# Optimization experiments

Hardware: AMD Instinct MI355X
Metric: run time of the kernel (lower is better)

Reference implementation:

```python
import jax, jax.numpy as jnp
import numpy as np

N = 5000
NFEAT = 512
NHID = 64
NHEADS = 8
NCLASS = 40
ALPHA = 0.2  # leaky relu slope
NEG_INF = -9e15


def setup_inputs() -> dict:
    key = jax.random.key(0)
    ks = jax.random.split(key, 12)
    x = jax.random.normal(ks[0], (N, NFEAT), dtype=jnp.float32)
    # binary adjacency, ~32 avg degree, with self loops
    adj = (jax.random.uniform(ks[1], (N, N)) < (32.0 / N)).astype(jnp.float32)
    adj = jnp.maximum(adj, jnp.eye(N, dtype=jnp.float32))
    s = 1.0 / np.sqrt(NFEAT)
    W_h = jax.random.uniform(ks[2], (NHEADS, NFEAT, NHID), minval=-s, maxval=s, dtype=jnp.float32)
    a_h = jax.random.uniform(ks[3], (NHEADS, 2 * NHID), minval=-s, maxval=s, dtype=jnp.float32)
    s2 = 1.0 / np.sqrt(NHID * NHEADS)
    W_o = jax.random.uniform(ks[4], (NHID * NHEADS, NHID), minval=-s2, maxval=s2, dtype=jnp.float32)
    a_o = jax.random.uniform(ks[5], (2 * NHID,), minval=-s2, maxval=s2, dtype=jnp.float32)
    s3 = 1.0 / np.sqrt(NHID)
    fc1_w = jax.random.uniform(ks[6], (NHID, 200), minval=-s3, maxval=s3, dtype=jnp.float32)
    fc1_b = jax.random.uniform(ks[7], (200,), minval=-s3, maxval=s3, dtype=jnp.float32)
    s4 = 1.0 / np.sqrt(200)
    fc2_w = jax.random.uniform(ks[8], (200, NCLASS), minval=-s4, maxval=s4, dtype=jnp.float32)
    fc2_b = jax.random.uniform(ks[9], (NCLASS,), minval=-s4, maxval=s4, dtype=jnp.float32)
    return {"x": x, "adj": adj, "W_h": W_h, "a_h": a_h, "W_o": W_o, "a_o": a_o,
            "fc1_w": fc1_w, "fc1_b": fc1_b, "fc2_w": fc2_w, "fc2_b": fc2_b}


def _masked_attention(e, adj):
    # e: [..., N, N]; mask where adj == 0, then row softmax
    e = jnp.where(adj > 0, e, NEG_INF)
    return jax.nn.softmax(e, axis=-1)


def reference(x, adj, W_h, a_h, W_o, a_o, fc1_w, fc1_b, fc2_w, fc2_b):
    # ---- multi-head GAT layer (concat=True), eval mode (dropout off) ----
    Wh = jnp.einsum('nf,hfo->hno', x, W_h)                 # [H, N, nhid]
    f1 = jnp.einsum('hno,ho->hn', Wh, a_h[:, :NHID])       # [H, N]
    f2 = jnp.einsum('hno,ho->hn', Wh, a_h[:, NHID:])       # [H, N]
    e = jax.nn.leaky_relu(f1[:, :, None] + f2[:, None, :], ALPHA)  # [H, N, N]
    att = _masked_attention(e, adj[None, :, :])
    h = jnp.einsum('hnm,hmo->hno', att, Wh)                # [H, N, nhid]
    h1 = jax.nn.elu(h).transpose(1, 0, 2).reshape(N, NHEADS * NHID)  # concat heads

    # ---- output GAT layer (concat=False) ----
    Wh2 = h1 @ W_o                                         # [N, nhid]
    g1 = Wh2 @ a_o[:NHID]                                  # [N]
    g2 = Wh2 @ a_o[NHID:]                                  # [N]
    e2 = jax.nn.leaky_relu(g1[:, None] + g2[None, :], ALPHA)
    att2 = _masked_attention(e2, adj)
    h2 = att2 @ Wh2                                        # [N, nhid]

    # ---- MLP head ----
    h3 = jax.nn.elu(h2 @ fc1_w + fc1_b)
    return h3 @ fc2_w + fc2_b                              # [N, nclass]
```

## Files before the change

kernel.cpp:

```cpp
#include <hip/hip_runtime.h>

typedef unsigned short u16;
typedef unsigned int u32;
typedef unsigned long long u64;
typedef __bf16 bf16_t;
typedef __bf16 bf16x8 __attribute__((ext_vector_type(8)));
typedef float f32x4 __attribute__((ext_vector_type(4)));

#define NN 5000
#define NF 512
#define NH 64
#define HEADS 8
#define NCLS 40
#define CAP 128
#define LRELU 0.2f

#define SCAN_BLKS 1250
#define CVT_AB_BLKS 344
#define PREP2_GRID (SCAN_BLKS + CVT_AB_BLKS + 8)

__device__ __forceinline__ bool adj_is_bf16(const void* adj) {
    return ((*(const u32*)adj) & 0xFFFFu) != 0u;
}
__device__ __forceinline__ u16 rne_bf16(float f) {
    u32 u = __float_as_uint(f);
    u += 0x7FFFu + ((u >> 16) & 1u);
    return (u16)(u >> 16);
}
__device__ __forceinline__ float up_bf16(u16 h) {
    return __uint_as_float((u32)h << 16);
}

__global__ __launch_bounds__(256) void prep2(const void* __restrict__ adj,
                                             const void* __restrict__ x, const void* __restrict__ W_h,
                                             const void* a_h, const void* W_o, const void* a_o,
                                             const void* f1w, const void* f1b,
                                             const void* f2w, const void* f2b,
                                             int* __restrict__ nbr, int* __restrict__ deg,
                                             u16* __restrict__ xc, u16* __restrict__ whc,
                                             float* a_hc, float* W_oc, float* a_oc,
                                             float* f1wc, float* f1bc, float* f2wc, float* f2bc) {
    const bool isb = adj_is_bf16(adj);
    const int b = blockIdx.x;
    if (b < SCAN_BLKS) {
        const int lane = threadIdx.x & 63;
        const int wid  = threadIdx.x >> 6;
        const int n = b * 4 + wid;
        int* nrow = nbr + (size_t)n * CAP;
        const u64 lt = (1ull << lane) - 1;
        int total = 0;
        if (!isb) {
            const uint4* row4 = (const uint4*)((const float*)adj + (size_t)n * NN);
            #pragma unroll
            for (int pass = 0; pass < 2; ++pass) {
                uint4 v[10];
                #pragma unroll
                for (int k = 0; k < 10; ++k) {
                    int c = (pass * 10 + k) * 64 + lane;
                    v[k] = (c < 1250) ? row4[c] : make_uint4(0u, 0u, 0u, 0u);
                }
                #pragma unroll
                for (int k = 0; k < 10; ++k) {
                    int c = (pass * 10 + k) * 64 + lane;
                    u32 w[4] = {v[k].x, v[k].y, v[k].z, v[k].w};
                    #pragma unroll
                    for (int j = 0; j < 4; ++j) {
                        bool nz = w[j] != 0u;
                        u64 m = __ballot(nz);
                        if (nz) {
                            int pos = total + __popcll(m & lt);
                            if (pos < CAP) nrow[pos] = c * 4 + j;
                        }
                        total += __popcll(m);
                    }
                }
            }
        } else {
            const uint4* row4 = (const uint4*)((const u16*)adj + (size_t)n * NN);
            #pragma unroll
            for (int pass = 0; pass < 2; ++pass) {
                uint4 v[5];
                #pragma unroll
                for (int k = 0; k < 5; ++k) {
                    int c = (pass * 5 + k) * 64 + lane;
                    v[k] = (c < 625) ? row4[c] : make_uint4(0u, 0u, 0u, 0u);
                }
                #pragma unroll
                for (int k = 0; k < 5; ++k) {
                    int c = (pass * 5 + k) * 64 + lane;
                    u32 w[4] = {v[k].x, v[k].y, v[k].z, v[k].w};
                    #pragma unroll
                    for (int j = 0; j < 4; ++j) {
                        bool nz = (w[j] & 0xFFFFu) != 0u;
                        u64 m = __ballot(nz);
                        if (nz) {
                            int pos = total + __popcll(m & lt);
                            if (pos < CAP) nrow[pos] = c * 8 + 2 * j;
                        }
                        total += __popcll(m);
                        bool nz2 = (w[j] >> 16) != 0u;
                        u64 m2 = __ballot(nz2);
                        if (nz2) {
                            int pos = total + __popcll(m2 & lt);
                            if (pos < CAP) nrow[pos] = c * 8 + 2 * j + 1;
                        }
                        total += __popcll(m2);
                    }
                }
            }
        }
        if (lane == 0) deg[n] = total < CAP ? total : CAP;
    } else if (b < SCAN_BLKS + CVT_AB_BLKS) {
        const int total = NN * NF + HEADS * NF * NH;
        for (int i = (b - SCAN_BLKS) * 256 + threadIdx.x; i < total; i += CVT_AB_BLKS * 256) {
            const void* src; u16* dst; int off;
            if (i < NN * NF) { src = x; dst = xc; off = i; }
            else             { src = W_h; dst = whc; off = i - NN * NF; }
            dst[off] = isb ? ((const u16*)src)[off] : rne_bf16(((const float*)src)[off]);
        }
    } else {
        const int s0 = HEADS * 2 * NH, s1 = HEADS * NH * NH, s2 = 2 * NH,
                  s3 = NH * 200, s4 = 200, s5 = 200 * NCLS, s6 = NCLS;
        const int total = s0 + s1 + s2 + s3 + s4 + s5 + s6;
        for (int i = (b - SCAN_BLKS - CVT_AB_BLKS) * 256 + threadIdx.x; i < total; i += 8 * 256) {
            const void* src; float* dst; int off = i;
            if (off < s0) { src = a_h; dst = a_hc; }
            else if ((off -= s0) < s1) { src = W_o;  dst = W_oc; }
            else if ((off -= s1) < s2) { src = a_o;  dst = a_oc; }
            else if ((off -= s2) < s3) { src = f1w;  dst = f1wc; }
            else if ((off -= s3) < s4) { src = f1b;  dst = f1bc; }
            else if ((off -= s4) < s5) { src = f2w;  dst = f2wc; }
            else { off -= s5;           src = f2b;  dst = f2bc; }
            dst[off] = isb ? up_bf16(((const u16*)src)[off]) : ((const float*)src)[off];
        }
    }
}

__global__ __launch_bounds__(256) void gemm1_f(const bf16_t* __restrict__ x,
                                               const bf16_t* __restrict__ W_h,
                                               const float* __restrict__ a_h,
                                               float* __restrict__ Wh,
                                               float* __restrict__ f1,
                                               float* __restrict__ f2) {
    const int lane = threadIdx.x & 63;
    const int wid  = threadIdx.x >> 6;
    const int rg = blockIdx.x;
    const int h  = blockIdx.y;
    const int quad = lane >> 4;
    const int lr   = lane & 15;
    const int kq   = quad * 8;
    const int nCol = wid * 16 + lr;
    const bf16_t* Bh = W_h + (size_t)h * NF * NH;
    __shared__ float f1s[4][64], f2s[4][64];

    bf16x8 bfrag[16];
    #pragma unroll
    for (int s = 0; s < 16; ++s) {
        bf16x8 bb;
        #pragma unroll
        for (int j = 0; j < 8; ++j) bb[j] = Bh[(s * 32 + kq + j) * NH + nCol];
        bfrag[s] = bb;
    }
    const float a1c = a_h[h * 128 + nCol];
    const float a2c = a_h[h * 128 + NH + nCol];

    for (int t = 0; t < 4; ++t) {
        const int rb = rg * 64 + t * 16;
        int row  = rb + lr;
        int rowc = row < NN ? row : NN - 1;
        const bf16_t* xp = x + (size_t)rowc * NF + kq;
        f32x4 acc = {0.f, 0.f, 0.f, 0.f};
        #pragma unroll
        for (int s = 0; s < 16; ++s) {
            bf16x8 a = *(const bf16x8*)(xp + s * 32);
            acc = __builtin_amdgcn_mfma_f32_16x16x32_bf16(a, bfrag[s], acc, 0, 0, 0);
        }
        #pragma unroll
        for (int r = 0; r < 4; ++r) {
            int gr = rb + quad * 4 + r;
            if (gr < NN) Wh[((size_t)(h * NN + gr)) * NH + nCol] = acc[r];
            float p1 = acc[r] * a1c, p2 = acc[r] * a2c;
            #pragma unroll
            for (int o = 8; o; o >>= 1) { p1 += __shfl_xor(p1, o); p2 += __shfl_xor(p2, o); }
            if (lr == 0) { f1s[wid][t * 16 + quad * 4 + r] = p1; f2s[wid][t * 16 + quad * 4 + r] = p2; }
        }
    }
    __syncthreads();
    if (wid == 0) {
        int gr = rg * 64 + lane;
        if (gr < NN) {
            f1[h * NN + gr] = f1s[0][lane] + f1s[1][lane] + f1s[2][lane] + f1s[3][lane];
            f2[h * NN + gr] = f2s[0][lane] + f2s[1][lane] + f2s[2][lane] + f2s[3][lane];
        }
    }
}

__global__ __launch_bounds__(256) void agg1(const float* __restrict__ Wh,
                                            const float* __restrict__ f1,
                                            const float* __restrict__ f2,
                                            const int* __restrict__ nbr,
                                            const int* __restrict__ deg,
                                            float* __restrict__ h1) {
    const int lane = threadIdx.x & 63;
    const int wid  = threadIdx.x >> 6;
    const int gw = blockIdx.x * 4 + wid;
    const int h = gw / NN;
    const int n = gw - h * NN;
    __shared__ float s_alpha[4][CAP];
    __shared__ int   s_nbr[4][CAP];
    const int d = deg[n];
    const int* nb = nbr + (size_t)n * CAP;
    const float f1n = f1[gw];
    const float* f2h = f2 + (size_t)h * NN;

    float mx = -INFINITY;
    for (int j = lane; j < d; j += 64) {
        int m = nb[j];
        s_nbr[wid][j] = m;
        float e = f1n + f2h[m];
        e = e > 0.f ? e : LRELU * e;
        s_alpha[wid][j] = e;
        mx = fmaxf(mx, e);
    }
    #pragma unroll
    for (int o = 32; o; o >>= 1) mx = fmaxf(mx, __shfl_xor(mx, o));
    float sm = 0.f;
    for (int j = lane; j < d; j += 64) {
        float p = expf(s_alpha[wid][j] - mx);
        s_alpha[wid][j] = p;
        sm += p;
    }
    #pragma unroll
    for (int o = 32; o; o >>= 1) sm += __shfl_xor(sm, o);

    float acc0 = 0.f, acc1 = 0.f, acc2 = 0.f, acc3 = 0.f;
    const float* WhL = Wh + (size_t)h * NN * NH + lane;
    int j = 0;
    for (; j + 4 <= d; j += 4) {
        acc0 += s_alpha[wid][j]     * WhL[(size_t)s_nbr[wid][j]     * NH];
        acc1 += s_alpha[wid][j + 1] * WhL[(size_t)s_nbr[wid][j + 1] * NH];
        acc2 += s_alpha[wid][j + 2] * WhL[(size_t)s_nbr[wid][j + 2] * NH];
        acc3 += s_alpha[wid][j + 3] * WhL[(size_t)s_nbr[wid][j + 3] * NH];
    }
    for (; j < d; ++j) acc0 += s_alpha[wid][j] * WhL[(size_t)s_nbr[wid][j] * NH];
    float hv = (acc0 + acc1 + acc2 + acc3) / sm;
    hv = hv > 0.f ? hv : expf(hv) - 1.f;
    h1[(size_t)n * (HEADS * NH) + h * NH + lane] = hv;
}

__global__ __launch_bounds__(256) void gemm2_4(const float* __restrict__ h1,
                                               const float* __restrict__ W_o,
                                               const float* __restrict__ a_o,
                                               float* __restrict__ Wh2,
                                               float* __restrict__ g1,
                                               float* __restrict__ g2) {
    const int t = threadIdx.x;
    const int n0 = blockIdx.x * 4;
    __shared__ float sh[4 * 512];
    __shared__ float ps[4][4][64];
    const float4* src = (const float4*)(h1 + (size_t)n0 * 512);
    ((float4*)sh)[t]       = src[t];
    ((float4*)sh)[t + 256] = src[t + 256];
    __syncthreads();
    const int o = t & 63, part = t >> 6;
    float a0 = 0.f, a1 = 0.f, a2 = 0.f, a3 = 0.f;
    const float* wo = W_o + part * 128 * 64 + o;
    const float* s0 = sh + part * 128;
    #pragma unroll 4
    for (int f = 0; f < 128; ++f) {
        float w = wo[f * 64];
        a0 += s0[f] * w; a1 += s0[512 + f] * w; a2 += s0[1024 + f] * w; a3 += s0[1536 + f] * w;
    }
    ps[part][0][o] = a0; ps[part][1][o] = a1; ps[part][2][o] = a2; ps[part][3][o] = a3;
    __syncthreads();
    const int nd = t >> 6;
    float w2 = ps[0][nd][o] + ps[1][nd][o] + ps[2][nd][o] + ps[3][nd][o];
    Wh2[(size_t)(n0 + nd) * 64 + o] = w2;
    float p1 = w2 * a_o[o], p2 = w2 * a_o[64 + o];
    #pragma unroll
    for (int s = 32; s; s >>= 1) { p1 += __shfl_xor(p1, s); p2 += __shfl_xor(p2, s); }
    if (o == 0) { g1[n0 + nd] = p1; g2[n0 + nd] = p2; }
}

__global__ __launch_bounds__(256) void agg2_mlp(const float* __restrict__ Wh2,
                                                const float* __restrict__ g1,
                                                const float* __restrict__ g2,
                                                const int* __restrict__ nbr,
                                                const int* __restrict__ deg,
                                                const float* __restrict__ fc1_w,
                                                const float* __restrict__ fc1_b,
                                                const float* __restrict__ fc2_w,
                                                const float* __restrict__ fc2_b,
                                                float* __restrict__ out) {
    const int lane = threadIdx.x & 63;
    const int wid  = threadIdx.x >> 6;
    const int t = threadIdx.x;
    const int n0 = blockIdx.x * 4;
    const int n = n0 + wid;
    __shared__ float s_alpha[4][CAP];
    __shared__ int   s_nbr[4][CAP];
    __shared__ float s_h2[4][NH];
    __shared__ float s_h3[4][200];
    __shared__ float ps2[2][4][NCLS];
    const int d = deg[n];
    const int* nb = nbr + (size_t)n * CAP;
    const float gn = g1[n];

    float mx = -INFINITY;
    for (int j = lane; j < d; j += 64) {
        int m = nb[j];
        s_nbr[wid][j] = m;
        float e = gn + g2[m];
        e = e > 0.f ? e : LRELU * e;
        s_alpha[wid][j] = e;
        mx = fmaxf(mx, e);
    }
    #pragma unroll
    for (int o = 32; o; o >>= 1) mx = fmaxf(mx, __shfl_xor(mx, o));
    float sm = 0.f;
    for (int j = lane; j < d; j += 64) {
        float p = expf(s_alpha[wid][j] - mx);
        s_alpha[wid][j] = p;
        sm += p;
    }
    #pragma unroll
    for (int o = 32; o; o >>= 1) sm += __shfl_xor(sm, o);

    float acc0 = 0.f, acc1 = 0.f, acc2 = 0.f, acc3 = 0.f;
    int j = 0;
    for (; j + 4 <= d; j += 4) {
        acc0 += s_alpha[wid][j]     * Wh2[(size_t)s_nbr[wid][j]     * NH + lane];
        acc1 += s_alpha[wid][j + 1] * Wh2[(size_t)s_nbr[wid][j + 1] * NH + lane];
        acc2 += s_alpha[wid][j + 2] * Wh2[(size_t)s_nbr[wid][j + 2] * NH + lane];
        acc3 += s_alpha[wid][j + 3] * Wh2[(size_t)s_nbr[wid][j + 3] * NH + lane];
    }
    for (; j < d; ++j) acc0 += s_alpha[wid][j] * Wh2[(size_t)s_nbr[wid][j] * NH + lane];
    s_h2[wid][lane] = (acc0 + acc1 + acc2 + acc3) / sm;
    __syncthreads();

    if (t < 200) {
        float b0 = 0.f, b1 = 0.f, b2 = 0.f, b3 = 0.f;
        #pragma unroll 4
        for (int f = 0; f < NH; ++f) {
            float w = fc1_w[f * 200 + t];
            b0 += s_h2[0][f] * w; b1 += s_h2[1][f] * w; b2 += s_h2[2][f] * w; b3 += s_h2[3][f] * w;
        }
        float bb = fc1_b[t];
        b0 += bb; b1 += bb; b2 += bb; b3 += bb;
        s_h3[0][t] = b0 > 0.f ? b0 : expf(b0) - 1.f;
        s_h3[1][t] = b1 > 0.f ? b1 : expf(b1) - 1.f;
        s_h3[2][t] = b2 > 0.f ? b2 : expf(b2) - 1.f;
        s_h3[3][t] = b3 > 0.f ? b3 : expf(b3) - 1.f;
    }
    __syncthreads();

    if (t < 80) {
        const int o = t % 40, fh = t / 40;
        float c0 = 0.f, c1 = 0.f, c2 = 0.f, c3 = 0.f;
        #pragma unroll 4
        for (int f = fh * 100; f < fh * 100 + 100; ++f) {
            float w = fc2_w[f * NCLS + o];
            c0 += s_h3[0][f] * w; c1 += s_h3[1][f] * w; c2 += s_h3[2][f] * w; c3 += s_h3[3][f] * w;
        }
        ps2[fh][0][o] = c0; ps2[fh][1][o] = c1; ps2[fh][2][o] = c2; ps2[fh][3][o] = c3;
    }
    __syncthreads();
    if (t < 160) {
        const int nd = t / 40, o = t % 40;
        out[(size_t)(n0 + nd) * NCLS + o] = ps2[0][nd][o] + ps2[1][nd][o] + fc2_b[o];
    }
}

extern "C" void kernel_launch(void* const* d_in, const int* in_sizes, int n_in,
                              void* d_out, int out_size, void* d_ws, size_t ws_size,
                              hipStream_t stream) {
    const void* x     = d_in[0];
    const void* adj   = d_in[1];
    const void* W_h   = d_in[2];
    const void* a_h   = d_in[3];
    const void* W_o   = d_in[4];
    const void* a_o   = d_in[5];
    const void* fc1_w = d_in[6];
    const void* fc1_b = d_in[7];
    const void* fc2_w = d_in[8];
    const void* fc2_b = d_in[9];
    float* out = (float*)d_out;

    char* ws = (char*)d_ws;
    int*   nbr   = (int*)(ws + 0);
    int*   deg   = (int*)(ws + 2560000);
    float* Wh    = (float*)(ws + 2580000);
    float* f1    = (float*)(ws + 12820000);
    float* f2    = (float*)(ws + 12980000);
    float* h1    = (float*)(ws + 13140000);
    float* Wh2   = (float*)(ws + 23380000);
    float* g1    = (float*)(ws + 24660000);
    float* g2    = (float*)(ws + 24680000);
    u16*   xc    = (u16*)(ws + 24700000);
    u16*   whc   = (u16*)(ws + 29820000);
    float* a_hc  = (float*)(ws + 30344288);
    float* W_oc  = (float*)(ws + 30348384);
    float* a_oc  = (float*)(ws + 30479456);
    float* f1wc  = (float*)(ws + 30479968);
    float* f1bc  = (float*)(ws + 30531168);
    float* f2wc  = (float*)(ws + 30531968);
    float* f2bc  = (float*)(ws + 30563968);

    prep2<<<PREP2_GRID, 256, 0, stream>>>(adj, x, W_h, a_h, W_o, a_o,
                                          fc1_w, fc1_b, fc2_w, fc2_b,
                                          nbr, deg, xc, whc, a_hc, W_oc, a_oc,
                                          f1wc, f1bc, f2wc, f2bc);
    gemm1_f<<<dim3(79, HEADS), 256, 0, stream>>>((const bf16_t*)xc, (const bf16_t*)whc,
                                                 a_hc, Wh, f1, f2);
    agg1<<<HEADS * NN / 4, 256, 0, stream>>>(Wh, f1, f2, nbr, deg, h1);
    gemm2_4<<<NN / 4, 256, 0, stream>>>(h1, W_oc, a_oc, Wh2, g1, g2);
    agg2_mlp<<<NN / 4, 256, 0, stream>>>(Wh2, g1, g2, nbr, deg,
                                         f1wc, f1bc, f2wc, f2bc, out);
}
```

Baseline: 283.2 us.

## Fuse adjacency scan into first-layer aggregation and vectorize input conversion

Moves the dense adjacency row scan out of the prep kernel and into the first-layer aggregation kernel. Each block now handles one node, with its four waves scanning quarters of the row and merging the neighbor lists in shared memory. Those lists are shared across all eight heads and still written to global memory for the second layer. The bf16 conversion of x and W_h now processes four elements per thread with nontemporal loads. The 100MB adjacency read now happens in a kernel that runs after the GEMM, which lengthens that kernel's critical path, and the node-per-block split leaves only two heads per wave.

Result: no change. 282.7 us (-0.2%).

```diff
diff --git a/kernel.cpp b/kernel.cpp
--- a/kernel.cpp
+++ b/kernel.cpp
@@ -6,6 +6,7 @@
 typedef __bf16 bf16_t;
 typedef __bf16 bf16x8 __attribute__((ext_vector_type(8)));
 typedef float f32x4 __attribute__((ext_vector_type(4)));
+typedef u32 u32x4 __attribute__((ext_vector_type(4)));
 
 #define NN 5000
 #define NF 512
@@ -15,9 +16,8 @@
 #define CAP 128
 #define LRELU 0.2f
 
-#define SCAN_BLKS 1250
-#define CVT_AB_BLKS 344
-#define PREP2_GRID (SCAN_BLKS + CVT_AB_BLKS + 8)
+#define CVT_BIG 320
+#define CVT_GRID (CVT_BIG + 8)
 
 __device__ __forceinline__ bool adj_is_bf16(const void* adj) {
     return ((*(const u32*)adj) & 0xFFFFu) != 0u;
@@ -30,99 +30,42 @@
 __device__ __forceinline__ float up_bf16(u16 h) {
     return __uint_as_float((u32)h << 16);
 }
-
-__global__ __launch_bounds__(256) void prep2(const void* __restrict__ adj,
-                                             const void* __restrict__ x, const void* __restrict__ W_h,
-                                             const void* a_h, const void* W_o, const void* a_o,
-                                             const void* f1w, const void* f1b,
-                                             const void* f2w, const void* f2b,
-                                             int* __restrict__ nbr, int* __restrict__ deg,
-                                             u16* __restrict__ xc, u16* __restrict__ whc,
-                                             float* a_hc, float* W_oc, float* a_oc,
-                                             float* f1wc, float* f1bc, float* f2wc, float* f2bc) {
+__device__ __forceinline__ u32x4 ntload4(const void* p, int idx) {
+    return __builtin_nontemporal_load(((const u32x4*)p) + idx);
+}
+
+__global__ __launch_bounds__(256) void cvt(const void* __restrict__ x, const void* __restrict__ W_h,
+                                           const void* __restrict__ adj,
+                                           const void* a_h, const void* W_o, const void* a_o,
+                                           const void* f1w, const void* f1b,
+                                           const void* f2w, const void* f2b,
+                                           u16* __restrict__ xc, u16* __restrict__ whc,
+                                           float* a_hc, float* W_oc, float* a_oc,
+                                           float* f1wc, float* f1bc, float* f2wc, float* f2bc) {
     const bool isb = adj_is_bf16(adj);
     const int b = blockIdx.x;
-    if (b < SCAN_BLKS) {
-        const int lane = threadIdx.x & 63;
-        const int wid  = threadIdx.x >> 6;
-        const int n = b * 4 + wid;
-        int* nrow = nbr + (size_t)n * CAP;
-        const u64 lt = (1ull << lane) - 1;
-        int total = 0;
-        if (!isb) {
-            const uint4* row4 = (const uint4*)((const float*)adj + (size_t)n * NN);
-            #pragma unroll
-            for (int pass = 0; pass < 2; ++pass) {
-                uint4 v[10];
-                #pragma unroll
-                for (int k = 0; k < 10; ++k) {
-                    int c = (pass * 10 + k) * 64 + lane;
-                    v[k] = (c < 1250) ? row4[c] : make_uint4(0u, 0u, 0u, 0u);
-                }
-                #pragma unroll
-                for (int k = 0; k < 10; ++k) {
-                    int c = (pass * 10 + k) * 64 + lane;
-                    u32 w[4] = {v[k].x, v[k].y, v[k].z, v[k].w};
-                    #pragma unroll
-                    for (int j = 0; j < 4; ++j) {
-                        bool nz = w[j] != 0u;
-                        u64 m = __ballot(nz);
-                        if (nz) {
-                            int pos = total + __popcll(m & lt);
-                            if (pos < CAP) nrow[pos] = c * 4 + j;
-                        }
-                        total += __popcll(m);
-                    }
-                }
+    if (b < CVT_BIG) {
+        const int X4 = NN * NF / 4;
+        const int T4 = X4 + HEADS * NF * NH / 4;
+        for (int i = b * 256 + threadIdx.x; i < T4; i += CVT_BIG * 256) {
+            const void* src; u16* dst; int off;
+            if (i < X4) { src = x; dst = xc; off = i; }
+            else        { src = W_h; dst = whc; off = i - X4; }
+            ushort4 o;
+            if (isb) {
+                o = ((const ushort4*)src)[off];
+            } else {
+                u32x4 vv = ntload4(src, off);
+                o.x = rne_bf16(__uint_as_float(vv[0])); o.y = rne_bf16(__uint_as_float(vv[1]));
+                o.z = rne_bf16(__uint_as_float(vv[2])); o.w = rne_bf16(__uint_as_float(vv[3]));
             }
-        } else {
-            const uint4* row4 = (const uint4*)((const u16*)adj + (size_t)n * NN);
-            #pragma unroll
-            for (int pass = 0; pass < 2; ++pass) {
-                uint4 v[5];
-                #pragma unroll
-                for (int k = 0; k < 5; ++k) {
-                    int c = (pass * 5 + k) * 64 + lane;
-                    v[k] = (c < 625) ? row4[c] : make_uint4(0u, 0u, 0u, 0u);
-                }
-                #pragma unroll
-                for (int k = 0; k < 5; ++k) {
-                    int c = (pass * 5 + k) * 64 + lane;
-                    u32 w[4] = {v[k].x, v[k].y, v[k].z, v[k].w};
-                    #pragma unroll
-                    for (int j = 0; j < 4; ++j) {
-                        bool nz = (w[j] & 0xFFFFu) != 0u;
-                        u64 m = __ballot(nz);
-                        if (nz) {
-                            int pos = total + __popcll(m & lt);
-                            if (pos < CAP) nrow[pos] = c * 8 + 2 * j;
-                        }
-                        total += __popcll(m);
-                        bool nz2 = (w[j] >> 16) != 0u;
-                        u64 m2 = __ballot(nz2);
-                        if (nz2) {
-                            int pos = total + __popcll(m2 & lt);
-                            if (pos < CAP) nrow[pos] = c * 8 + 2 * j + 1;
-                        }
-                        total += __popcll(m2);
-                    }
-                }
-            }
-        }
-        if (lane == 0) deg[n] = total < CAP ? total : CAP;
-    } else if (b < SCAN_BLKS + CVT_AB_BLKS) {
-        const int total = NN * NF + HEADS * NF * NH;
-        for (int i = (b - SCAN_BLKS) * 256 + threadIdx.x; i < total; i += CVT_AB_BLKS * 256) {
-            const void* src; u16* dst; int off;
-            if (i < NN * NF) { src = x; dst = xc; off = i; }
-            else             { src = W_h; dst = whc; off = i - NN * NF; }
-            dst[off] = isb ? ((const u16*)src)[off] : rne_bf16(((const float*)src)[off]);
+            ((ushort4*)dst)[off] = o;
         }
     } else {
         const int s0 = HEADS * 2 * NH, s1 = HEADS * NH * NH, s2 = 2 * NH,
                   s3 = NH * 200, s4 = 200, s5 = 200 * NCLS, s6 = NCLS;
         const int total = s0 + s1 + s2 + s3 + s4 + s5 + s6;
-        for (int i = (b - SCAN_BLKS - CVT_AB_BLKS) * 256 + threadIdx.x; i < total; i += 8 * 256) {
+        for (int i = (b - CVT_BIG) * 256 + threadIdx.x; i < total; i += 8 * 256) {
             const void* src; float* dst; int off = i;
             if (off < s0) { src = a_h; dst = a_hc; }
             else if ((off -= s0) < s1) { src = W_o;  dst = W_oc; }
@@ -195,57 +138,111 @@
     }
 }
 
-__global__ __launch_bounds__(256) void agg1(const float* __restrict__ Wh,
-                                            const float* __restrict__ f1,
-                                            const float* __restrict__ f2,
-                                            const int* __restrict__ nbr,
-                                            const int* __restrict__ deg,
-                                            float* __restrict__ h1) {
+__global__ __launch_bounds__(256) void agg1f(const void* __restrict__ adj,
+                                             const float* __restrict__ Wh,
+                                             const float* __restrict__ f1,
+                                             const float* __restrict__ f2,
+                                             int* __restrict__ nbr, int* __restrict__ deg,
+                                             float* __restrict__ h1) {
+    const bool isb = adj_is_bf16(adj);
     const int lane = threadIdx.x & 63;
     const int wid  = threadIdx.x >> 6;
-    const int gw = blockIdx.x * 4 + wid;
-    const int h = gw / NN;
-    const int n = gw - h * NN;
-    __shared__ float s_alpha[4][CAP];
-    __shared__ int   s_nbr[4][CAP];
-    const int d = deg[n];
-    const int* nb = nbr + (size_t)n * CAP;
-    const float f1n = f1[gw];
-    const float* f2h = f2 + (size_t)h * NN;
-
-    float mx = -INFINITY;
-    for (int j = lane; j < d; j += 64) {
-        int m = nb[j];
-        s_nbr[wid][j] = m;
-        float e = f1n + f2h[m];
-        e = e > 0.f ? e : LRELU * e;
-        s_alpha[wid][j] = e;
-        mx = fmaxf(mx, e);
-    }
+    const int n = blockIdx.x;
+    __shared__ int   s_seg[4][CAP];
+    __shared__ int   s_cnt[4];
+    __shared__ int   s_nbr[CAP];
+    __shared__ float s_alpha[HEADS][CAP];
+    const u64 lt = (1ull << lane) - 1;
+
+    int total = 0;
+    if (!isb) {
+        const float* row = (const float*)adj + (size_t)n * NN;
+        const int c0 = wid * 313, cend = min(1250, c0 + 313);
+        for (int base = c0; base < cend; base += 64) {
+            int c = base + lane;
+            u32x4 v = {0u, 0u, 0u, 0u};
+            if (c < cend) v = ntload4(row, c);
+            #pragma unroll
+            for (int j = 0; j < 4; ++j) {
+                bool nz = v[j] != 0u;
+                u64 m = __ballot(nz);
+                if (nz) { int pos = total + __popcll(m & lt); if (pos < CAP) s_seg[wid][pos] = c * 4 + j; }
+                total += __popcll(m);
+            }
+        }
+    } else {
+        const u16* row = (const u16*)adj + (size_t)n * NN;
+        const int c0 = wid * 157, cend = min(625, c0 + 157);
+        for (int base = c0; base < cend; base += 64) {
+            int c = base + lane;
+            u32x4 v = {0u, 0u, 0u, 0u};
+            if (c < cend) v = ntload4(row, c);
+            #pragma unroll
+            for (int j = 0; j < 4; ++j) {
+                bool nz = (v[j] & 0xFFFFu) != 0u;
+                u64 m = __ballot(nz);
+                if (nz) { int pos = total + __popcll(m & lt); if (pos < CAP) s_seg[wid][pos] = c * 8 + 2 * j; }
+                total += __popcll(m);
+                bool nz2 = (v[j] >> 16) != 0u;
+                u64 m2 = __ballot(nz2);
+                if (nz2) { int pos = total + __popcll(m2 & lt); if (pos < CAP) s_seg[wid][pos] = c * 8 + 2 * j + 1; }
+                total += __popcll(m2);
+            }
+        }
+    }
+    if (lane == 0) s_cnt[wid] = total < CAP ? total : CAP;
+    __syncthreads();
+    const int c0_ = s_cnt[0], c1_ = s_cnt[1], c2_ = s_cnt[2], c3_ = s_cnt[3];
+    const int offw = (wid > 0 ? c0_ : 0) + (wid > 1 ? c1_ : 0) + (wid > 2 ? c2_ : 0);
+    const int dall0 = c0_ + c1_ + c2_ + c3_;
+    const int dall = dall0 < CAP ? dall0 : CAP;
+    for (int i = lane; i < s_cnt[wid]; i += 64) {
+        int p = offw + i;
+        if (p < CAP) s_nbr[p] = s_seg[wid][i];
+    }
+    __syncthreads();
+    for (int i = threadIdx.x; i < dall; i += 256) nbr[(size_t)n * CAP + i] = s_nbr[i];
+    if (threadIdx.x == 0) deg[n] = dall;
+
     #pragma unroll
-    for (int o = 32; o; o >>= 1) mx = fmaxf(mx, __shfl_xor(mx, o));
-    float sm = 0.f;
-    for (int j = lane; j < d; j += 64) {
-        float p = expf(s_alpha[wid][j] - mx);
-        s_alpha[wid][j] = p;
-        sm += p;
-    }
-    #pragma unroll
-    for (int o = 32; o; o >>= 1) sm += __shfl_xor(sm, o);
-
-    float acc0 = 0.f, acc1 = 0.f, acc2 = 0.f, acc3 = 0.f;
-    const float* WhL = Wh + (size_t)h * NN * NH + lane;
-    int j = 0;
-    for (; j + 4 <= d; j += 4) {
-        acc0 += s_alpha[wid][j]     * WhL[(size_t)s_nbr[wid][j]     * NH];
-        acc1 += s_alpha[wid][j + 1] * WhL[(size_t)s_nbr[wid][j + 1] * NH];
-        acc2 += s_alpha[wid][j + 2] * WhL[(size_t)s_nbr[wid][j + 2] * NH];
-        acc3 += s_alpha[wid][j + 3] * WhL[(size_t)s_nbr[wid][j + 3] * NH];
-    }
-    for (; j < d; ++j) acc0 += s_alpha[wid][j] * WhL[(size_t)s_nbr[wid][j] * NH];
-    float hv = (acc0 + acc1 + acc2 + acc3) / sm;
-    hv = hv > 0.f ? hv : expf(hv) - 1.f;
-    h1[(size_t)n * (HEADS * NH) + h * NH + lane] = hv;
+    for (int rep = 0; rep < 2; ++rep) {
+        const int h = wid + rep * 4;
+        const float f1n = f1[h * NN + n];
+        const float* f2h = f2 + (size_t)h * NN;
+        float e0 = -INFINITY, e1 = -INFINITY;
+        if (lane < dall) {
+            float e = f1n + f2h[s_nbr[lane]];
+            e0 = e > 0.f ? e : LRELU * e;
+        }
+        if (lane + 64 < dall) {
+            float e = f1n + f2h[s_nbr[lane + 64]];
+            e1 = e > 0.f ? e : LRELU * e;
+        }
+        float mx = fmaxf(e0, e1);
+        #pragma unroll
+        for (int o = 32; o; o >>= 1) mx = fmaxf(mx, __shfl_xor(mx, o));
+        float p0 = lane < dall ? expf(e0 - mx) : 0.f;
+        float p1 = lane + 64 < dall ? expf(e1 - mx) : 0.f;
+        float sm = p0 + p1;
+        #pragma unroll
+        for (int o = 32; o; o >>= 1) sm += __shfl_xor(sm, o);
+        s_alpha[h][lane] = p0;
+        s_alpha[h][lane + 64] = p1;
+
+        float acc0 = 0.f, acc1 = 0.f, acc2 = 0.f, acc3 = 0.f;
+        const float* WhL = Wh + (size_t)h * NN * NH + lane;
+        int j = 0;
+        for (; j + 4 <= dall; j += 4) {
+            acc0 += s_alpha[h][j]     * WhL[(size_t)s_nbr[j]     * NH];
+            acc1 += s_alpha[h][j + 1] * WhL[(size_t)s_nbr[j + 1] * NH];
+            acc2 += s_alpha[h][j + 2] * WhL[(size_t)s_nbr[j + 2] * NH];
+            acc3 += s_alpha[h][j + 3] * WhL[(size_t)s_nbr[j + 3] * NH];
+        }
+        for (; j < dall; ++j) acc0 += s_alpha[h][j] * WhL[(size_t)s_nbr[j] * NH];
+        float hv = (acc0 + acc1 + acc2 + acc3) / sm;
+        hv = hv > 0.f ? hv : expf(hv) - 1.f;
+        h1[(size_t)n * (HEADS * NH) + h * NH + lane] = hv;
+    }
 }
 
 __global__ __launch_bounds__(256) void gemm2_4(const float* __restrict__ h1,
@@ -406,13 +403,13 @@
     float* f2wc  = (float*)(ws + 30531968);
     float* f2bc  = (float*)(ws + 30563968);
 
-    prep2<<<PREP2_GRID, 256, 0, stream>>>(adj, x, W_h, a_h, W_o, a_o,
-                                          fc1_w, fc1_b, fc2_w, fc2_b,
-                                          nbr, deg, xc, whc, a_hc, W_oc, a_oc,
-                                          f1wc, f1bc, f2wc, f2bc);
+    cvt<<<CVT_GRID, 256, 0, stream>>>(x, W_h, adj, a_h, W_o, a_o,
+                                      fc1_w, fc1_b, fc2_w, fc2_b,
+                                      xc, whc, a_hc, W_oc, a_oc,
+                                      f1wc, f1bc, f2wc, f2bc);
     gemm1_f<<<dim3(79, HEADS), 256, 0, stream>>>((const bf16_t*)xc, (const bf16_t*)whc,
                                                  a_hc, Wh, f1, f2);
-    agg1<<<HEADS * NN / 4, 256, 0, stream>>>(Wh, f1, f2, nbr, deg, h1);
+    agg1f<<<NN, 256, 0, stream>>>(adj, Wh, f1, f2, nbr, deg, h1);
     gemm2_4<<<NN / 4, 256, 0, stream>>>(h1, W_oc, a_oc, Wh2, g1, g2);
     agg2_mlp<<<NN / 4, 256, 0, stream>>>(Wh2, g1, g2, nbr, deg,
                                          f1wc, f1bc, f2wc, f2bc, out);
```
